# Kernel optimization log

Hardware: AMD Instinct MI355X
Metric: run time of the kernel (lower is better)

The kernel has to match this reference:

```python
import jax, jax.numpy as jnp
import numpy as np

B, L, D = 2, 1024, 512
E = 2
DI = E * D            # d_inner = 1024
N = 16                # d_state
K = 4                 # d_conv
DT_RANK = 32          # ceil(d_model / 16)


def setup_inputs() -> dict:
    key = jax.random.key(0)
    ks = jax.random.split(key, 12)
    s = lambda i, shape, scale=0.02: jax.random.normal(ks[i], shape, jnp.float32) * scale
    return {
        "x": jax.random.normal(ks[0], (B, L, D), jnp.float32),
        # Mamba params (mamba_ssm layout: Linear weights are [out, in])
        "W_in": s(1, (2 * DI, D)),                 # in_proj, bias=False
        "conv_w": s(2, (DI, K), 0.1),              # depthwise conv kernel
        "conv_b": jnp.zeros((DI,), jnp.float32),
        "W_xproj": s(3, (DT_RANK + 2 * N, DI)),    # x_proj, bias=False
        "W_dt": s(4, (DI, DT_RANK), 0.1),
        "b_dt": s(5, (DI,), 0.5),
        "A_log": jnp.log(jnp.broadcast_to(jnp.arange(1, N + 1, dtype=jnp.float32), (DI, N))),
        "D_skip": jnp.ones((DI,), jnp.float32),
        "W_out": s(6, (D, DI)),                    # out_proj, bias=False
        # block params
        "g1": jnp.ones((D,), jnp.float32), "b1": jnp.zeros((D,), jnp.float32),
        "W_ff1": s(7, (2 * D, D)), "b_ff1": jnp.zeros((2 * D,), jnp.float32),
        "W_ff2": s(8, (D, 2 * D)), "b_ff2": jnp.zeros((D,), jnp.float32),
        "g2": jnp.ones((D,), jnp.float32), "b2": jnp.zeros((D,), jnp.float32),
    }


def layernorm(x, g, b, eps=1e-5):
    m = x.mean(-1, keepdims=True)
    v = jnp.mean(jnp.square(x - m), -1, keepdims=True)
    return (x - m) * jax.lax.rsqrt(v + eps) * g + b


def mamba(x, W_in, conv_w, conv_b, W_xproj, W_dt, b_dt, A_log, D_skip, W_out):
    xz = x @ W_in.T                              # [B,L,2*DI]
    u, z = jnp.split(xz, 2, axis=-1)             # each [B,L,DI]
    # causal depthwise conv1d over time
    u_t = u.transpose(0, 2, 1)                   # [B,DI,L]
    conv = jax.lax.conv_general_dilated(
        u_t, conv_w[:, None, :], (1,), [(K - 1, 0)], feature_group_count=DI)
    u = jax.nn.silu(conv.transpose(0, 2, 1) + conv_b)   # [B,L,DI]
    # input-dependent dt, B, C
    x_dbl = u @ W_xproj.T                        # [B,L,DT_RANK+2N]
    dt_r, Bm, Cm = jnp.split(x_dbl, [DT_RANK, DT_RANK + N], axis=-1)
    dt = jax.nn.softplus(dt_r @ W_dt.T + b_dt)   # [B,L,DI]
    A = -jnp.exp(A_log)                          # [DI,N]
    dA = jnp.exp(dt[..., None] * A)                                # [B,L,DI,N]
    dBu = dt[..., None] * Bm[:, :, None, :] * u[..., None]         # [B,L,DI,N]

    def step(h, xs):
        dA_t, dBu_t, C_t = xs
        h = dA_t * h + dBu_t                    # [B,DI,N]
        y = jnp.einsum('bdn,bn->bd', h, C_t)
        return h, y

    h0 = jnp.zeros((B, DI, N), dt.dtype)
    _, ys = jax.lax.scan(step, h0, (dA.transpose(1, 0, 2, 3),
                                    dBu.transpose(1, 0, 2, 3),
                                    Cm.transpose(1, 0, 2)))
    y = ys.transpose(1, 0, 2) + u * D_skip       # [B,L,DI]
    y = y * jax.nn.silu(z)
    return y @ W_out.T                            # [B,L,D]


def reference(x, W_in, conv_w, conv_b, W_xproj, W_dt, b_dt, A_log, D_skip, W_out,
              g1, b1, W_ff1, b_ff1, W_ff2, b_ff2, g2, b2):
    m = mamba(x, W_in, conv_w, conv_b, W_xproj, W_dt, b_dt, A_log, D_skip, W_out)
    res1 = x - m
    r = layernorm(res1, g1, b1)
    ff = jax.nn.gelu(r @ W_ff1.T + b_ff1, approximate=False) @ W_ff2.T + b_ff2
    res2 = r - ff
    out = layernorm(jax.nn.silu(res2), g2, b2)
    return out + x
```

## Files before the change

kernel.cpp:

```cpp
#include <hip/hip_runtime.h>
#include <math.h>

#define BB 2
#define LL 1024
#define DD 512
#define DIN 1024
#define NS 16
#define RNK 32
#define ML (BB*LL)
#define CT 16
#define NC (LL/CT)
#define BDIN (BB*DIN)

typedef unsigned short u16;
typedef unsigned int u32;

__device__ __forceinline__ float sigmoidf_(float v) { return 1.f / (1.f + __expf(-v)); }
__device__ __forceinline__ float siluf_(float v) { return v * sigmoidf_(v); }
__device__ __forceinline__ u16 f2bf(float f) {
  union { float f; u32 u; } c; c.f = f;
  u32 r = c.u + 0x7fffu + ((c.u >> 16) & 1u);
  return (u16)(r >> 16);
}
__device__ __forceinline__ float bf2f(u16 x) {
  union { u32 u; float f; } c; c.u = (u32)x << 16;
  return c.f;
}

template<typename T>
__device__ __forceinline__ uint4 ld8bf(const T* p);
template<> __device__ __forceinline__ uint4 ld8bf<u16>(const u16* p) {
  return *(const uint4*)p;
}
template<> __device__ __forceinline__ uint4 ld8bf<float>(const float* p) {
  float4 v0 = *(const float4*)p;
  float4 v1 = *(const float4*)(p + 4);
  union { u16 u[8]; uint4 v; } q;
  q.u[0] = f2bf(v0.x); q.u[1] = f2bf(v0.y); q.u[2] = f2bf(v0.z); q.u[3] = f2bf(v0.w);
  q.u[4] = f2bf(v1.x); q.u[5] = f2bf(v1.y); q.u[6] = f2bf(v1.z); q.u[7] = f2bf(v1.w);
  return q.v;
}

using bf16x8 = __attribute__((ext_vector_type(8))) short;
using f32x4  = __attribute__((ext_vector_type(4))) float;

template<int BM, int BN, int BK, int EPI, typename OT, typename TA, typename TW>
__global__ __launch_bounds__(256) void gemm_t(const TA* __restrict__ A,
                                              const TW* __restrict__ W,
                                              const float* __restrict__ bias,
                                              OT* __restrict__ C,
                                              int M, int N, int K)
{
  constexpr int WR = BM / 64;
  constexpr int WC = 4 / WR;
  constexpr int NW = BN / WC;
  constexpr int JJ = NW / 16;
  constexpr int RB = BN / 64;
  constexpr int KK = BK / 32;
  __shared__ u16 As[BM][BK + 8];
  __shared__ u16 Bs[BN][BK + 8];
  const int bm = blockIdx.y * BM, bn = blockIdx.x * BN;
  const int tid = threadIdx.x;
  const int w = tid >> 6, l = tid & 63;
  const int wr = w / WC, wc = w % WC;
  const int lr = l & 15, lh = l >> 4;
  const int sr0 = tid >> 2, sc0 = tid & 3;
  f32x4 acc[4][JJ] = {};
  for (int k0 = 0; k0 < K; k0 += BK) {
    uint4 areg[WR][KK], breg[RB][KK];
#pragma unroll
    for (int i = 0; i < WR; ++i)
#pragma unroll
      for (int kk = 0; kk < KK; ++kk)
        areg[i][kk] = ld8bf(&A[(size_t)(bm + sr0 + 64 * i) * K + k0 + kk * 32 + sc0 * 8]);
#pragma unroll
    for (int i = 0; i < RB; ++i)
#pragma unroll
      for (int kk = 0; kk < KK; ++kk)
        breg[i][kk] = ld8bf(&W[(size_t)(bn + sr0 + 64 * i) * K + k0 + kk * 32 + sc0 * 8]);
    __syncthreads();
#pragma unroll
    for (int i = 0; i < WR; ++i)
#pragma unroll
      for (int kk = 0; kk < KK; ++kk)
        *(uint4*)&As[sr0 + 64 * i][kk * 32 + sc0 * 8] = areg[i][kk];
#pragma unroll
    for (int i = 0; i < RB; ++i)
#pragma unroll
      for (int kk = 0; kk < KK; ++kk)
        *(uint4*)&Bs[sr0 + 64 * i][kk * 32 + sc0 * 8] = breg[i][kk];
    __syncthreads();
    bf16x8 af[KK][4], bfr[KK][JJ];
#pragma unroll
    for (int kk = 0; kk < KK; ++kk) {
#pragma unroll
      for (int i = 0; i < 4; ++i)  af[kk][i]  = *(bf16x8*)&As[wr * 64 + i * 16 + lr][kk * 32 + lh * 8];
#pragma unroll
      for (int j = 0; j < JJ; ++j) bfr[kk][j] = *(bf16x8*)&Bs[wc * NW + j * 16 + lr][kk * 32 + lh * 8];
    }
#pragma unroll
    for (int kk = 0; kk < KK; ++kk)
#pragma unroll
      for (int i = 0; i < 4; ++i)
#pragma unroll
        for (int j = 0; j < JJ; ++j)
          acc[i][j] = __builtin_amdgcn_mfma_f32_16x16x32_bf16(af[kk][i], bfr[kk][j], acc[i][j], 0, 0, 0);
  }
#pragma unroll
  for (int i = 0; i < 4; ++i) {
#pragma unroll
    for (int j = 0; j < JJ; ++j) {
      int col = bn + wc * NW + j * 16 + lr;
      float bv = (EPI >= 1) ? bias[col] : 0.f;
#pragma unroll
      for (int r = 0; r < 4; ++r) {
        int row = bm + wr * 64 + i * 16 + lh * 4 + r;
        float t = acc[i][j][r] + bv;
        if (EPI == 2) t = 0.5f * t * (1.f + erff(t * 0.70710678118654752f));
        if (EPI == 3) t = fmaxf(t, 0.f) + log1pf(__expf(-fabsf(t)));
        if constexpr (sizeof(OT) == 2) C[(size_t)row * N + col] = (OT)f2bf(t);
        else                           C[(size_t)row * N + col] = (OT)t;
      }
    }
  }
}

__global__ __launch_bounds__(256) void xproj_mfma(const u16* __restrict__ A,
                                                  const float* __restrict__ W,
                                                  float* __restrict__ C,
                                                  u16* __restrict__ bdtr)
{
  __shared__ u16 As[128][40];
  __shared__ u16 Bs[64][40];
  const int bm = blockIdx.x * 128;
  const int tid = threadIdx.x;
  const int w = tid >> 6, l = tid & 63;
  const int lr = l & 15, lh = l >> 4;
  const int sr0 = tid >> 2, sc0 = tid & 3;
  f32x4 acc[2][4] = {};
  for (int k0 = 0; k0 < DIN; k0 += 32) {
    uint4 a0 = ld8bf(&A[(size_t)(bm + sr0) * DIN + k0 + sc0 * 8]);
    uint4 a1 = ld8bf(&A[(size_t)(bm + sr0 + 64) * DIN + k0 + sc0 * 8]);
    uint4 b0;
    if (sr0 < 64) b0 = ld8bf(&W[(size_t)sr0 * DIN + k0 + sc0 * 8]);
    __syncthreads();
    *(uint4*)&As[sr0][sc0 * 8] = a0;
    *(uint4*)&As[sr0 + 64][sc0 * 8] = a1;
    if (sr0 < 64) *(uint4*)&Bs[sr0][sc0 * 8] = b0;
    __syncthreads();
    bf16x8 af[2], bfr[4];
#pragma unroll
    for (int i = 0; i < 2; ++i) af[i]  = *(bf16x8*)&As[w * 32 + i * 16 + lr][lh * 8];
#pragma unroll
    for (int j = 0; j < 4; ++j) bfr[j] = *(bf16x8*)&Bs[j * 16 + lr][lh * 8];
#pragma unroll
    for (int i = 0; i < 2; ++i)
#pragma unroll
      for (int j = 0; j < 4; ++j)
        acc[i][j] = __builtin_amdgcn_mfma_f32_16x16x32_bf16(af[i], bfr[j], acc[i][j], 0, 0, 0);
  }
#pragma unroll
  for (int i = 0; i < 2; ++i)
#pragma unroll
    for (int j = 0; j < 4; ++j) {
      int col = j * 16 + lr;
#pragma unroll
      for (int r = 0; r < 4; ++r) {
        int row = bm + w * 32 + i * 16 + lh * 4 + r;
        float v = acc[i][j][r];
        C[(size_t)row * 64 + col] = v;
        if (j < 2) bdtr[(size_t)row * RNK + col] = f2bf(v);
      }
    }
}

__global__ __launch_bounds__(256) void conv_silu8(const u16* __restrict__ xzb,
                                                  const float* __restrict__ conv_w,
                                                  const float* __restrict__ conv_b,
                                                  u16* __restrict__ ucb)
{
  int gid = blockIdx.x * 256 + threadIdx.x;
  int d8 = (gid & (DIN / 8 - 1)) * 8;
  int bl = gid >> 7;
  int l = bl & (LL - 1);
  int b = bl >> 10;
  float acc[8];
  {
    float4 c0 = *(const float4*)&conv_b[d8];
    float4 c1 = *(const float4*)&conv_b[d8 + 4];
    acc[0] = c0.x; acc[1] = c0.y; acc[2] = c0.z; acc[3] = c0.w;
    acc[4] = c1.x; acc[5] = c1.y; acc[6] = c1.z; acc[7] = c1.w;
  }
  float4 wv[8];
#pragma unroll
  for (int j = 0; j < 8; ++j) wv[j] = *(const float4*)&conv_w[(d8 + j) * 4];
#pragma unroll
  for (int k = 0; k < 4; ++k) {
    int ls = l - 3 + k;
    if (ls >= 0) {
      const u16* p = &xzb[((size_t)(b * LL + ls)) * (2 * DIN) + d8];
      ushort4 a0 = *(const ushort4*)p;
      ushort4 a1 = *(const ushort4*)(p + 4);
      float xv[8] = { bf2f(a0.x), bf2f(a0.y), bf2f(a0.z), bf2f(a0.w),
                      bf2f(a1.x), bf2f(a1.y), bf2f(a1.z), bf2f(a1.w) };
      const float* wk = (const float*)wv;
#pragma unroll
      for (int j = 0; j < 8; ++j) acc[j] = fmaf(xv[j], wk[j * 4 + k], acc[j]);
    }
  }
  union { u16 u[8]; uint4 v; } o;
#pragma unroll
  for (int j = 0; j < 8; ++j) o.u[j] = f2bf(siluf_(acc[j]));
  *(uint4*)&ucb[(size_t)bl * DIN + d8] = o.v;
}


__global__ __launch_bounds__(256) void scan_p1(const u16* __restrict__ dtb,
                                               const u16* __restrict__ ucb,
                                               const float* __restrict__ xdbl,
                                               const float* __restrict__ A_log,
                                               float* __restrict__ apG,
                                               float* __restrict__ hG)
{
  __shared__ float dts[CT][256];
  __shared__ float us[CT][256];
  __shared__ float Bs[CT][NS];
  const int d0 = blockIdx.x * 256, c = blockIdx.y, b = blockIdx.z;
  const int tid = threadIdx.x;
  const int t0 = c * CT;
  for (int i = tid; i < CT * 64; i += 256) {
    int r = i >> 6, col = (i & 63) * 4;
    size_t row = (size_t)(b * LL + t0 + r);
    ushort4 dv = *(const ushort4*)&dtb[row * DIN + d0 + col];
    float4 df = { bf2f(dv.x), bf2f(dv.y), bf2f(dv.z), bf2f(dv.w) };
    *(float4*)&dts[r][col] = df;
    ushort4 uv = *(const ushort4*)&ucb[row * DIN + d0 + col];
    float4 uf = { bf2f(uv.x), bf2f(uv.y), bf2f(uv.z), bf2f(uv.w) };
    *(float4*)&us[r][col] = uf;
  }
  { int r = tid >> 4, n = tid & 15;
    Bs[r][n] = xdbl[(size_t)(b * LL + t0 + r) * 64 + 32 + n]; }
  __syncthreads();
  const int d = d0 + tid;
  float Ad[NS];
#pragma unroll
  for (int n = 0; n < NS; ++n) Ad[n] = -__expf(A_log[d * NS + n]);
  float h[NS] = {};
  float sdt = 0.f;
#pragma unroll 4
  for (int t = 0; t < CT; ++t) {
    float dtv = dts[t][tid];
    float dtu = dtv * us[t][tid];
    sdt += dtv;
    float4 B0 = *(float4*)&Bs[t][0],  B1 = *(float4*)&Bs[t][4];
    float4 B2 = *(float4*)&Bs[t][8],  B3 = *(float4*)&Bs[t][12];
    float Bq[NS] = { B0.x, B0.y, B0.z, B0.w, B1.x, B1.y, B1.z, B1.w,
                     B2.x, B2.y, B2.z, B2.w, B3.x, B3.y, B3.z, B3.w };
#pragma unroll
    for (int n = 0; n < NS; ++n) {
      float a = __expf(dtv * Ad[n]);
      h[n] = fmaf(a, h[n], dtu * Bq[n]);
    }
  }
  const int bd = b * DIN + d;
#pragma unroll
  for (int n = 0; n < NS; ++n) {
    apG[((size_t)c * NS + n) * BDIN + bd] = __expf(Ad[n] * sdt);
    hG [((size_t)c * NS + n) * BDIN + bd] = h[n];
  }
}

__global__ __launch_bounds__(128) void scan_p2(const float* __restrict__ apG,
                                               float* __restrict__ hG)
{
  const int idx = blockIdx.x * 128 + threadIdx.x;
  float H = 0.f;
#pragma unroll 16
  for (int c = 0; c < NC; ++c) {
    size_t o = (size_t)c * (NS * BDIN) + idx;
    float ap = apG[o];
    float hl = hG[o];
    hG[o] = H;
    H = fmaf(ap, H, hl);
  }
}

__global__ __launch_bounds__(256) void scan_p3(const u16* __restrict__ dtb,
                                               const u16* __restrict__ ucb,
                                               const u16* __restrict__ xzb,
                                               const float* __restrict__ xdbl,
                                               const float* __restrict__ A_log,
                                               const float* __restrict__ D_skip,
                                               const float* __restrict__ hG,
                                               u16* __restrict__ ygb)
{
  __shared__ float dts[CT][256];
  __shared__ float us[CT][256];
  __shared__ float zs[CT][256];
  __shared__ float Bs[CT][NS];
  __shared__ float Cs[CT][NS];
  const int d0 = blockIdx.x * 256, c = blockIdx.y, b = blockIdx.z;
  const int tid = threadIdx.x;
  const int t0 = c * CT;
  for (int i = tid; i < CT * 64; i += 256) {
    int r = i >> 6, col = (i & 63) * 4;
    size_t row = (size_t)(b * LL + t0 + r);
    ushort4 dv = *(const ushort4*)&dtb[row * DIN + d0 + col];
    float4 df = { bf2f(dv.x), bf2f(dv.y), bf2f(dv.z), bf2f(dv.w) };
    *(float4*)&dts[r][col] = df;
    ushort4 uv = *(const ushort4*)&ucb[row * DIN + d0 + col];
    float4 uf = { bf2f(uv.x), bf2f(uv.y), bf2f(uv.z), bf2f(uv.w) };
    *(float4*)&us[r][col] = uf;
    ushort4 zv = *(const ushort4*)&xzb[row * (2 * DIN) + DIN + d0 + col];
    float4 zf = { bf2f(zv.x), bf2f(zv.y), bf2f(zv.z), bf2f(zv.w) };
    *(float4*)&zs[r][col] = zf;
  }
  { int r = tid >> 4, n = tid & 15;
    size_t row = (size_t)(b * LL + t0 + r);
    Bs[r][n] = xdbl[row * 64 + 32 + n];
    Cs[r][n] = xdbl[row * 64 + 48 + n]; }
  __syncthreads();
  const int d = d0 + tid;
  const int bd = b * DIN + d;
  float Ad[NS];
#pragma unroll
  for (int n = 0; n < NS; ++n) Ad[n] = -__expf(A_log[d * NS + n]);
  const float Dd = D_skip[d];
  float h[NS];
#pragma unroll
  for (int n = 0; n < NS; ++n) h[n] = hG[((size_t)c * NS + n) * BDIN + bd];
#pragma unroll 2
  for (int t = 0; t < CT; ++t) {
    float dtv = dts[t][tid];
    float ucv = us[t][tid];
    float dtu = dtv * ucv;
    float4 B0 = *(float4*)&Bs[t][0],  B1 = *(float4*)&Bs[t][4];
    float4 B2 = *(float4*)&Bs[t][8],  B3 = *(float4*)&Bs[t][12];
    float4 C0 = *(float4*)&Cs[t][0],  C1 = *(float4*)&Cs[t][4];
    float4 C2 = *(float4*)&Cs[t][8],  C3 = *(float4*)&Cs[t][12];
    float Bq[NS] = { B0.x, B0.y, B0.z, B0.w, B1.x, B1.y, B1.z, B1.w,
                     B2.x, B2.y, B2.z, B2.w, B3.x, B3.y, B3.z, B3.w };
    float Cq[NS] = { C0.x, C0.y, C0.z, C0.w, C1.x, C1.y, C1.z, C1.w,
                     C2.x, C2.y, C2.z, C2.w, C3.x, C3.y, C3.z, C3.w };
    float y = 0.f;
#pragma unroll
    for (int n = 0; n < NS; ++n) {
      float a = __expf(dtv * Ad[n]);
      h[n] = fmaf(a, h[n], dtu * Bq[n]);
      y = fmaf(h[n], Cq[n], y);
    }
    float o = fmaf(ucv, Dd, y) * siluf_(zs[t][tid]);
    ygb[(size_t)(b * LL + t0 + t) * DIN + d0 + tid] = f2bf(o);
  }
}

__global__ __launch_bounds__(256) void ln1_kernel(const float* __restrict__ x,
                                                  const float* __restrict__ m,
                                                  const float* __restrict__ g,
                                                  const float* __restrict__ b,
                                                  float* __restrict__ r,
                                                  u16* __restrict__ rbf)
{
  int row = blockIdx.x;
  int tid = threadIdx.x;
  size_t base = (size_t)row * DD;
  float2 xv = *(const float2*)&x[base + tid * 2];
  float2 mv = *(const float2*)&m[base + tid * 2];
  float v0 = xv.x - mv.x, v1 = xv.y - mv.y;
  float s = v0 + v1, ss = v0 * v0 + v1 * v1;
#pragma unroll
  for (int off = 32; off; off >>= 1) { s += __shfl_down(s, off, 64); ss += __shfl_down(ss, off, 64); }
  __shared__ float sm[8];
  int w = tid >> 6;
  if ((tid & 63) == 0) { sm[w] = s; sm[4 + w] = ss; }
  __syncthreads();
  float S = sm[0] + sm[1] + sm[2] + sm[3];
  float SS = sm[4] + sm[5] + sm[6] + sm[7];
  float mean = S * (1.f / DD);
  float var = SS * (1.f / DD) - mean * mean;
  float rstd = rsqrtf(var + 1e-5f);
  float2 gv = *(const float2*)&g[tid * 2];
  float2 bv = *(const float2*)&b[tid * 2];
  float2 o;
  o.x = (v0 - mean) * rstd * gv.x + bv.x;
  o.y = (v1 - mean) * rstd * gv.y + bv.y;
  *(float2*)&r[base + tid * 2] = o;
  u32 pk = (u32)f2bf(o.x) | ((u32)f2bf(o.y) << 16);
  *(u32*)&rbf[base + tid * 2] = pk;
}

__global__ __launch_bounds__(256) void final_kernel(const float* __restrict__ r,
                                                    const float* __restrict__ ff,
                                                    const float* __restrict__ x,
                                                    const float* __restrict__ g,
                                                    const float* __restrict__ b,
                                                    float* __restrict__ out)
{
  int row = blockIdx.x;
  int tid = threadIdx.x;
  size_t base = (size_t)row * DD;
  float2 rv = *(const float2*)&r[base + tid * 2];
  float2 fv = *(const float2*)&ff[base + tid * 2];
  float v0 = rv.x - fv.x, v1 = rv.y - fv.y;
  v0 = siluf_(v0); v1 = siluf_(v1);
  float s = v0 + v1, ss = v0 * v0 + v1 * v1;
#pragma unroll
  for (int off = 32; off; off >>= 1) { s += __shfl_down(s, off, 64); ss += __shfl_down(ss, off, 64); }
  __shared__ float sm[8];
  int w = tid >> 6;
  if ((tid & 63) == 0) { sm[w] = s; sm[4 + w] = ss; }
  __syncthreads();
  float S = sm[0] + sm[1] + sm[2] + sm[3];
  float SS = sm[4] + sm[5] + sm[6] + sm[7];
  float mean = S * (1.f / DD);
  float var = SS * (1.f / DD) - mean * mean;
  float rstd = rsqrtf(var + 1e-5f);
  float2 gv = *(const float2*)&g[tid * 2];
  float2 bv = *(const float2*)&b[tid * 2];
  float2 xv = *(const float2*)&x[base + tid * 2];
  float2 o;
  o.x = (v0 - mean) * rstd * gv.x + bv.x + xv.x;
  o.y = (v1 - mean) * rstd * gv.y + bv.y + xv.y;
  *(float2*)&out[base + tid * 2] = o;
}

extern "C" void kernel_launch(void* const* d_in, const int* in_sizes, int n_in,
                              void* d_out, int out_size, void* d_ws, size_t ws_size,
                              hipStream_t stream)
{
  const float* x      = (const float*)d_in[0];
  const float* W_in   = (const float*)d_in[1];
  const float* conv_w = (const float*)d_in[2];
  const float* conv_b = (const float*)d_in[3];
  const float* W_xp   = (const float*)d_in[4];
  const float* W_dt   = (const float*)d_in[5];
  const float* b_dt   = (const float*)d_in[6];
  const float* A_log  = (const float*)d_in[7];
  const float* D_skip = (const float*)d_in[8];
  const float* W_out  = (const float*)d_in[9];
  const float* g1     = (const float*)d_in[10];
  const float* b1     = (const float*)d_in[11];
  const float* W_ff1  = (const float*)d_in[12];
  const float* b_ff1  = (const float*)d_in[13];
  const float* W_ff2  = (const float*)d_in[14];
  const float* b_ff2  = (const float*)d_in[15];
  const float* g2     = (const float*)d_in[16];
  const float* b2     = (const float*)d_in[17];
  float* out = (float*)d_out;

  float* ws = (float*)d_ws;
  u16*   xzb  = (u16*)ws;
  float* xdbl = ws + 2097152;
  u16*   dtb  = (u16*)(ws + 2228224);
  float* apG  = ws + 3276800;
  float* hG   = ws + 5373952;
  float* mb   = ws + 7471104;
  float* rb   = ws + 8519680;
  u16*   bffh = (u16*)(ws + 9568256);
  u16*   ygb  = (u16*)(ws + 10616832);
  u16*   ucb  = (u16*)(ws + 11665408);
  u16*   brb  = (u16*)(ws + 12713984);
  u16*   bdtr = (u16*)(ws + 13238272);

  gemm_t<128, 64, 64, 0, u16, float, float><<<dim3(2 * DIN / 64, ML / 128), 256, 0, stream>>>(
      x, W_in, nullptr, xzb, ML, 2 * DIN, DD);
  conv_silu8<<<(ML * DIN / 8) / 256, 256, 0, stream>>>(xzb, conv_w, conv_b, ucb);
  xproj_mfma<<<ML / 128, 256, 0, stream>>>(ucb, W_xp, xdbl, bdtr);
  gemm_t<128, 64, 32, 3, u16, u16, float><<<dim3(DIN / 64, ML / 128), 256, 0, stream>>>(
      bdtr, W_dt, b_dt, dtb, ML, DIN, RNK);
  scan_p1<<<dim3(DIN / 256, NC, BB), 256, 0, stream>>>(dtb, ucb, xdbl, A_log, apG, hG);
  scan_p2<<<(NS * BDIN) / 128, 128, 0, stream>>>(apG, hG);
  scan_p3<<<dim3(DIN / 256, NC, BB), 256, 0, stream>>>(dtb, ucb, xzb, xdbl, A_log, D_skip,
                                                       hG, ygb);
  gemm_t<64, 64, 64, 0, float, u16, float><<<dim3(DD / 64, ML / 64), 256, 0, stream>>>(
      ygb, W_out, nullptr, mb, ML, DD, DIN);
  ln1_kernel<<<ML, 256, 0, stream>>>(x, mb, g1, b1, rb, brb);
  gemm_t<128, 64, 64, 2, u16, u16, float><<<dim3(DIN / 64, ML / 128), 256, 0, stream>>>(
      brb, W_ff1, b_ff1, bffh, ML, DIN, DD);
  gemm_t<64, 64, 64, 1, float, u16, float><<<dim3(DD / 64, ML / 64), 256, 0, stream>>>(
      bffh, W_ff2, b_ff2, mb, ML, DD, DIN);
  final_kernel<<<ML, 256, 0, stream>>>(rb, mb, x, g2, b2, out);
}
```

Baseline: 159.9 us.

## Fuse dt projection and softplus into scan kernels, drop dt GEMM

Removes the separate rank-32 dt GEMM launch and its bf16 dt buffer. Each scan thread now loads its 32 W_dt weights into registers, reads the chunk's dt_r rows into shared memory, and computes dt plus softplus on the fly in both scan passes. This saves one launch and the write and read of a [B*L, DI] intermediate. In exchange the dt computation runs twice (p1 and p3), and each thread holds 32 extra registers, which may lower occupancy.

```diff
diff --git a/kernel.cpp b/kernel.cpp
--- a/kernel.cpp
+++ b/kernel.cpp
@@ -117,7 +117,6 @@
         int row = bm + wr * 64 + i * 16 + lh * 4 + r;
         float t = acc[i][j][r] + bv;
         if (EPI == 2) t = 0.5f * t * (1.f + erff(t * 0.70710678118654752f));
-        if (EPI == 3) t = fmaxf(t, 0.f) + log1pf(__expf(-fabsf(t)));
         if constexpr (sizeof(OT) == 2) C[(size_t)row * N + col] = (OT)f2bf(t);
         else                           C[(size_t)row * N + col] = (OT)t;
       }
@@ -215,25 +214,58 @@
 }
 
 
-__global__ __launch_bounds__(256) void scan_p1(const u16* __restrict__ dtb,
+__device__ __forceinline__ void load_dt_inputs(const u16* __restrict__ bdtr,
+                                               const float* __restrict__ W_dt,
+                                               const float* __restrict__ b_dt,
+                                               int b, int t0, int d, int tid,
+                                               u16 (*dtr_s)[RNK], float* wdt, float& bdtd)
+{
+  if (tid < CT * RNK / 4) {
+    int r = tid >> 3, cq = (tid & 7) * 4;
+    *(ushort4*)&dtr_s[r][cq] = *(const ushort4*)&bdtr[(size_t)(b * LL + t0 + r) * RNK + cq];
+  }
+#pragma unroll
+  for (int q = 0; q < RNK / 4; ++q) {
+    float4 wv = *(const float4*)&W_dt[(size_t)d * RNK + q * 4];
+    wdt[q * 4 + 0] = bf2f(f2bf(wv.x));
+    wdt[q * 4 + 1] = bf2f(f2bf(wv.y));
+    wdt[q * 4 + 2] = bf2f(f2bf(wv.z));
+    wdt[q * 4 + 3] = bf2f(f2bf(wv.w));
+  }
+  bdtd = b_dt[d];
+}
+
+__device__ __forceinline__ float dt_at(const u16 (*dtr_s)[RNK], const float* wdt,
+                                       float bdtd, int t)
+{
+  float a = bdtd;
+#pragma unroll
+  for (int k = 0; k < RNK; ++k) a = fmaf(bf2f(dtr_s[t][k]), wdt[k], a);
+  float sp = fmaxf(a, 0.f) + log1pf(__expf(-fabsf(a)));
+  return bf2f(f2bf(sp));
+}
+
+__global__ __launch_bounds__(256) void scan_p1(const u16* __restrict__ bdtr,
                                                const u16* __restrict__ ucb,
                                                const float* __restrict__ xdbl,
                                                const float* __restrict__ A_log,
+                                               const float* __restrict__ W_dt,
+                                               const float* __restrict__ b_dt,
                                                float* __restrict__ apG,
                                                float* __restrict__ hG)
 {
-  __shared__ float dts[CT][256];
   __shared__ float us[CT][256];
   __shared__ float Bs[CT][NS];
+  __shared__ u16 dtr_s[CT][RNK];
   const int d0 = blockIdx.x * 256, c = blockIdx.y, b = blockIdx.z;
   const int tid = threadIdx.x;
   const int t0 = c * CT;
+  const int d = d0 + tid;
+  float wdt[RNK]; float bdtd;
+  load_dt_inputs(bdtr, W_dt, b_dt, b, t0, d, tid, dtr_s, wdt, bdtd);
   for (int i = tid; i < CT * 64; i += 256) {
     int r = i >> 6, col = (i & 63) * 4;
     size_t row = (size_t)(b * LL + t0 + r);
-    ushort4 dv = *(const ushort4*)&dtb[row * DIN + d0 + col];
-    float4 df = { bf2f(dv.x), bf2f(dv.y), bf2f(dv.z), bf2f(dv.w) };
-    *(float4*)&dts[r][col] = df;
     ushort4 uv = *(const ushort4*)&ucb[row * DIN + d0 + col];
     float4 uf = { bf2f(uv.x), bf2f(uv.y), bf2f(uv.z), bf2f(uv.w) };
     *(float4*)&us[r][col] = uf;
@@ -241,7 +273,6 @@
   { int r = tid >> 4, n = tid & 15;
     Bs[r][n] = xdbl[(size_t)(b * LL + t0 + r) * 64 + 32 + n]; }
   __syncthreads();
-  const int d = d0 + tid;
   float Ad[NS];
 #pragma unroll
   for (int n = 0; n < NS; ++n) Ad[n] = -__expf(A_log[d * NS + n]);
@@ -249,7 +280,7 @@
   float sdt = 0.f;
 #pragma unroll 4
   for (int t = 0; t < CT; ++t) {
-    float dtv = dts[t][tid];
+    float dtv = dt_at(dtr_s, wdt, bdtd, t);
     float dtu = dtv * us[t][tid];
     sdt += dtv;
     float4 B0 = *(float4*)&Bs[t][0],  B1 = *(float4*)&Bs[t][4];
@@ -285,29 +316,31 @@
   }
 }
 
-__global__ __launch_bounds__(256) void scan_p3(const u16* __restrict__ dtb,
+__global__ __launch_bounds__(256) void scan_p3(const u16* __restrict__ bdtr,
                                                const u16* __restrict__ ucb,
                                                const u16* __restrict__ xzb,
                                                const float* __restrict__ xdbl,
                                                const float* __restrict__ A_log,
+                                               const float* __restrict__ W_dt,
+                                               const float* __restrict__ b_dt,
                                                const float* __restrict__ D_skip,
                                                const float* __restrict__ hG,
                                                u16* __restrict__ ygb)
 {
-  __shared__ float dts[CT][256];
   __shared__ float us[CT][256];
   __shared__ float zs[CT][256];
   __shared__ float Bs[CT][NS];
   __shared__ float Cs[CT][NS];
+  __shared__ u16 dtr_s[CT][RNK];
   const int d0 = blockIdx.x * 256, c = blockIdx.y, b = blockIdx.z;
   const int tid = threadIdx.x;
   const int t0 = c * CT;
+  const int d = d0 + tid;
+  float wdt[RNK]; float bdtd;
+  load_dt_inputs(bdtr, W_dt, b_dt, b, t0, d, tid, dtr_s, wdt, bdtd);
   for (int i = tid; i < CT * 64; i += 256) {
     int r = i >> 6, col = (i & 63) * 4;
     size_t row = (size_t)(b * LL + t0 + r);
-    ushort4 dv = *(const ushort4*)&dtb[row * DIN + d0 + col];
-    float4 df = { bf2f(dv.x), bf2f(dv.y), bf2f(dv.z), bf2f(dv.w) };
-    *(float4*)&dts[r][col] = df;
     ushort4 uv = *(const ushort4*)&ucb[row * DIN + d0 + col];
     float4 uf = { bf2f(uv.x), bf2f(uv.y), bf2f(uv.z), bf2f(uv.w) };
     *(float4*)&us[r][col] = uf;
@@ -320,7 +353,6 @@
     Bs[r][n] = xdbl[row * 64 + 32 + n];
     Cs[r][n] = xdbl[row * 64 + 48 + n]; }
   __syncthreads();
-  const int d = d0 + tid;
   const int bd = b * DIN + d;
   float Ad[NS];
 #pragma unroll
@@ -331,7 +363,7 @@
   for (int n = 0; n < NS; ++n) h[n] = hG[((size_t)c * NS + n) * BDIN + bd];
 #pragma unroll 2
   for (int t = 0; t < CT; ++t) {
-    float dtv = dts[t][tid];
+    float dtv = dt_at(dtr_s, wdt, bdtd, t);
     float ucv = us[t][tid];
     float dtu = dtv * ucv;
     float4 B0 = *(float4*)&Bs[t][0],  B1 = *(float4*)&Bs[t][4];
@@ -451,7 +483,6 @@
   float* ws = (float*)d_ws;
   u16*   xzb  = (u16*)ws;
   float* xdbl = ws + 2097152;
-  u16*   dtb  = (u16*)(ws + 2228224);
   float* apG  = ws + 3276800;
   float* hG   = ws + 5373952;
   float* mb   = ws + 7471104;
@@ -466,12 +497,11 @@
       x, W_in, nullptr, xzb, ML, 2 * DIN, DD);
   conv_silu8<<<(ML * DIN / 8) / 256, 256, 0, stream>>>(xzb, conv_w, conv_b, ucb);
   xproj_mfma<<<ML / 128, 256, 0, stream>>>(ucb, W_xp, xdbl, bdtr);
-  gemm_t<128, 64, 32, 3, u16, u16, float><<<dim3(DIN / 64, ML / 128), 256, 0, stream>>>(
-      bdtr, W_dt, b_dt, dtb, ML, DIN, RNK);
-  scan_p1<<<dim3(DIN / 256, NC, BB), 256, 0, stream>>>(dtb, ucb, xdbl, A_log, apG, hG);
+  scan_p1<<<dim3(DIN / 256, NC, BB), 256, 0, stream>>>(bdtr, ucb, xdbl, A_log, W_dt, b_dt,
+                                                       apG, hG);
   scan_p2<<<(NS * BDIN) / 128, 128, 0, stream>>>(apG, hG);
-  scan_p3<<<dim3(DIN / 256, NC, BB), 256, 0, stream>>>(dtb, ucb, xzb, xdbl, A_log, D_skip,
-                                                       hG, ygb);
+  scan_p3<<<dim3(DIN / 256, NC, BB), 256, 0, stream>>>(bdtr, ucb, xzb, xdbl, A_log, W_dt,
+                                                       b_dt, D_skip, hG, ygb);
   gemm_t<64, 64, 64, 0, float, u16, float><<<dim3(DD / 64, ML / 64), 256, 0, stream>>>(
       ygb, W_out, nullptr, mb, ML, DD, DIN);
   ln1_kernel<<<ML, 256, 0, stream>>>(x, mb, g1, b1, rb, brb);
```

Measured after the change: 173.7 us. +8.6%, slower.
